# Kernel optimization log

Hardware: AMD Instinct MI355X
Metric: run time of the kernel (lower is better)

## Reference

```python
import jax, jax.numpy as jnp
import numpy as np

P, U, R, C = 100000, 20000, 1000, 500
D, T, B = 64, 50, 4096
ET = 50000
NNZ_COL, NNZ_REG, NNZ_CAT, NNZ_T = 1_000_000, 300_000, 300_000, 1_000_000
N_LAYERS = 2


def setup_inputs() -> dict:
    key = jax.random.key(0)
    ks = iter(jax.random.split(key, 64))
    def nrm(shape, s=0.05):
        return (jax.random.normal(next(ks), shape, jnp.float32) * s)
    def ridx(n, hi):
        return jax.random.randint(next(ks), (n,), 0, hi, dtype=jnp.int32)
    def vals(n, scale):
        # roughly degree-normalized positive incidence weights
        return jax.random.uniform(next(ks), (n,), jnp.float32) * scale
    inp = {
        'user_idx': ridx(B, U),
        'user_seq': ridx((B, T)[0] * T, P + 1).reshape(B, T),
        'user_seq_mask': jax.random.randint(next(ks), (B, T), 0, 2, dtype=jnp.int32),
        'col_poi_idx': ridx(NNZ_COL, P), 'col_user_idx': ridx(NNZ_COL, U),
        'col_vals_pe': vals(NNZ_COL, 0.02), 'col_vals_ep': vals(NNZ_COL, 0.1),
        'reg_poi_idx': ridx(NNZ_REG, P), 'reg_region_idx': ridx(NNZ_REG, R),
        'reg_vals_pe': vals(NNZ_REG, 0.005), 'reg_vals_ep': vals(NNZ_REG, 0.3),
        'cat_poi_idx': ridx(NNZ_CAT, P), 'cat_cat_idx': ridx(NNZ_CAT, C),
        'cat_vals_pe': vals(NNZ_CAT, 0.003), 'cat_vals_ep': vals(NNZ_CAT, 0.3),
        'trans_poi_idx': ridx(NNZ_T, P), 'trans_edge_idx': ridx(NNZ_T, ET),
        'trans_vals_tar': vals(NNZ_T, 0.05), 'trans_vals_src': vals(NNZ_T, 0.1),
        'poi_emb': nrm((P + 1, D)), 'user_emb': nrm((U, D)),
        'region_emb': nrm((R, D)), 'cat_emb': nrm((C, D)),
        'w_gate_col': nrm((D, D)), 'b_gate_col': nrm((1, D)),
        'w_gate_trans': nrm((D, D)), 'b_gate_trans': nrm((1, D)),
        'w_gate_reg': nrm((D, D)), 'b_gate_reg': nrm((1, D)),
        'w_gate_cat': nrm((D, D)), 'b_gate_cat': nrm((1, D)),
        'col_Wp': nrm((D, D)), 'col_We': nrm((D, D)), 'col_Wf': nrm((2 * D, D)),
        'reg_Wp': nrm((D, D)), 'reg_We': nrm((D, D)), 'reg_Wf': nrm((2 * D, D)),
        'cat_Wp': nrm((D, D)), 'cat_We': nrm((D, D)), 'cat_Wf': nrm((2 * D, D)),
    }
    return inp


def _spmm(rows, cols, vals, X, n_rows):
    # sparse[n_rows, n_cols] @ X : gather source rows, scale, scatter-add to dest
    return jax.ops.segment_sum(vals[:, None] * X[cols], rows, num_segments=n_rows)


def _gate(x, W, b):
    return x * jax.nn.sigmoid(x @ W + b)


def _hetero_net(poi, edge, poi_idx, edge_idx, vals_pe, vals_ep, Wp, We, Wf, n_edge):
    # HG_poi_to_edge: rows=edge_idx, cols=poi_idx ; HG_edge_to_poi: rows=poi_idx, cols=edge_idx
    n_poi = poi.shape[0]
    acc_p, acc_e = poi, edge
    p, e = poi, edge
    for _ in range(N_LAYERS):
        poi_msg = _spmm(edge_idx, poi_idx, vals_pe, p @ Wp, n_edge)   # [n_edge, D]
        fused = jnp.concatenate([poi_msg, e @ We], axis=1) @ Wf       # [n_edge, D]
        prop = _spmm(poi_idx, edge_idx, vals_ep, fused, n_poi)        # [n_poi, D]
        p = prop + p      # residual (dropout p=0 -> identity)
        e = fused + e
        acc_p = acc_p + p
        acc_e = acc_e + e
    inv = 1.0 / (N_LAYERS + 1)
    return acc_p * inv, acc_e * inv


def _directed_net(poi, poi_idx, edge_idx, vals_tar, vals_src):
    n_poi = poi.shape[0]
    acc = poi
    p = poi
    for _ in range(N_LAYERS):
        msg_tar = _spmm(edge_idx, poi_idx, vals_tar, p, ET)       # HG_poi_tar @ p
        msg_src = _spmm(poi_idx, edge_idx, vals_src, msg_tar, n_poi)  # HG_poi_src @ msg_tar
        p = msg_src + p
        acc = acc + p
    return acc / (N_LAYERS + 1)


def _masked_mean(seq_embs, mask):
    m = mask.astype(seq_embs.dtype)[..., None]  # [B,T,1]
    denom = jnp.clip(m.sum(axis=1), 1.0)
    return (seq_embs * m).sum(axis=1) / denom


def reference(user_idx, user_seq, user_seq_mask,
              col_poi_idx, col_user_idx, col_vals_pe, col_vals_ep,
              reg_poi_idx, reg_region_idx, reg_vals_pe, reg_vals_ep,
              cat_poi_idx, cat_cat_idx, cat_vals_pe, cat_vals_ep,
              trans_poi_idx, trans_edge_idx, trans_vals_tar, trans_vals_src,
              poi_emb, user_emb, region_emb, cat_emb,
              w_gate_col, b_gate_col, w_gate_trans, b_gate_trans,
              w_gate_reg, b_gate_reg, w_gate_cat, b_gate_cat,
              col_Wp, col_We, col_Wf, reg_Wp, reg_We, reg_Wf,
              cat_Wp, cat_We, cat_Wf):
    base = poi_emb[:-1]  # drop padding row, [P, D]
    col_p = _gate(base, w_gate_col, b_gate_col)
    trans_p = _gate(base, w_gate_trans, b_gate_trans)
    reg_p = _gate(base, w_gate_reg, b_gate_reg)
    cat_p = _gate(base, w_gate_cat, b_gate_cat)

    col_poi_out, col_user_out = _hetero_net(col_p, user_emb, col_poi_idx, col_user_idx,
                                            col_vals_pe, col_vals_ep, col_Wp, col_We, col_Wf, U)
    reg_poi_out, _ = _hetero_net(reg_p, region_emb, reg_poi_idx, reg_region_idx,
                                 reg_vals_pe, reg_vals_ep, reg_Wp, reg_We, reg_Wf, R)
    cat_poi_out, _ = _hetero_net(cat_p, cat_emb, cat_poi_idx, cat_cat_idx,
                                 cat_vals_pe, cat_vals_ep, cat_Wp, cat_We, cat_Wf, C)
    trans_poi_out = _directed_net(trans_p, trans_poi_idx, trans_edge_idx,
                                  trans_vals_tar, trans_vals_src)

    zero = jnp.zeros((1, D), base.dtype)
    col_pad = jnp.concatenate([col_poi_out, zero], axis=0)
    reg_pad = jnp.concatenate([reg_poi_out, zero], axis=0)
    cat_pad = jnp.concatenate([cat_poi_out, zero], axis=0)
    trans_pad = jnp.concatenate([trans_poi_out, zero], axis=0)

    col_u = col_user_out[user_idx] + _masked_mean(col_pad[user_seq], user_seq_mask)
    reg_u = _masked_mean(reg_pad[user_seq], user_seq_mask)
    cat_u = _masked_mean(cat_pad[user_seq], user_seq_mask)
    trans_u = _masked_mean(trans_pad[user_seq], user_seq_mask)

    return jnp.stack([col_u, trans_u, reg_u, cat_u])  # [4, B, D]


if __name__ == '__main__':
    out = reference(**setup_inputs())
    print(out.shape, out.dtype)
```

## Files before the change

### kernel.cpp

```cpp
#include <hip/hip_runtime.h>

#define D 64
constexpr int Pn  = 100000;
constexpr int Un  = 20000;
constexpr int Rn  = 1000;
constexpr int Cn  = 500;
constexpr int Tn  = 50;
constexpr int Bn  = 4096;
constexpr int ETn = 50000;
constexpr int NNZ_COL = 1000000;
constexpr int NNZ_REG = 300000;
constexpr int NNZ_CAT = 300000;
constexpr int NNZ_T   = 1000000;
constexpr int STILE = 7040;
constexpr int NBMAX = 1024;
constexpr int CAP2 = 1536;
constexpr int NB2  = (Pn + 127) / 128;

static inline int cdiv(int a, int b) { return (a + b - 1) / b; }

__device__ __forceinline__ unsigned short f2bf(float f) {
  unsigned u = __float_as_uint(f);
  unsigned r = (u + 0x7FFF + ((u >> 16) & 1)) >> 16;
  return (unsigned short)r;
}
__device__ __forceinline__ float bflo(unsigned d) {
  return __uint_as_float(d << 16);
}
__device__ __forceinline__ float bfhi(unsigned d) {
  return __uint_as_float(d & 0xFFFF0000u);
}
__device__ __forceinline__ unsigned packbf(float a, float b) {
  return (unsigned)f2bf(a) | ((unsigned)f2bf(b) << 16);
}

struct SG {
  const int* k1; const int* o1; const float* v1;
  const int* k2; const int* o2; const float* v2;
  int2* sd; int* rowptr; int* cursorB;
  int s1, nb1, nk1, cap1, nblk, nnz, tile0, bkt0;
};
struct SG4 { SG g[4]; };

__global__ __launch_bounds__(256) void gate_kernel(
    const float* __restrict__ Xin, const float* __restrict__ W,
    const float* __restrict__ bias, unsigned short* __restrict__ P16,
    unsigned short* __restrict__ A16, int N) {
  __shared__ float sx[4][D];
  int tid = threadIdx.x, wv = tid >> 6, lane = tid & 63;
  float wcol[D];
#pragma unroll
  for (int k = 0; k < D; ++k) wcol[k] = W[k * D + lane];
  float bl = bias[lane];
  for (int row = blockIdx.x * 4 + wv; row < N; row += gridDim.x * 4) {
    float x = Xin[row * D + lane];
    sx[wv][lane] = x;
    float y = 0.f;
#pragma unroll
    for (int k = 0; k < D; ++k) y += sx[wv][k] * wcol[k];
    float s = 1.f / (1.f + __expf(-(y + bl)));
    float o = x * s;
    unsigned short ob = f2bf(o);
    P16[row * D + lane] = ob;
    A16[row * D + lane] = ob;
  }
}

__global__ __launch_bounds__(256) void matmul_kernel(
    const float* __restrict__ Xin, const float* __restrict__ W,
    float* __restrict__ Y, int N) {
  __shared__ float sx[4][D];
  int tid = threadIdx.x, wv = tid >> 6, lane = tid & 63;
  float wcol[D];
#pragma unroll
  for (int k = 0; k < D; ++k) wcol[k] = W[k * D + lane];
  for (int row = blockIdx.x * 4 + wv; row < N; row += gridDim.x * 4) {
    sx[wv][lane] = Xin[row * D + lane];
    float y = 0.f;
#pragma unroll
    for (int k = 0; k < D; ++k) y += sx[wv][k] * wcol[k];
    Y[row * D + lane] = y;
  }
}

__global__ __launch_bounds__(256) void fused2_resid_kernel(
    const float* __restrict__ A, const float* __restrict__ W1,
    const float* __restrict__ W2, unsigned short* __restrict__ fusedOut16,
    float* __restrict__ e_buf, float* __restrict__ accE, int N) {
  __shared__ float sa[4][D], sb2[4][D];
  int tid = threadIdx.x, wv = tid >> 6, lane = tid & 63;
  float w1[D], w2[D];
#pragma unroll
  for (int k = 0; k < D; ++k) {
    w1[k] = W1[k * D + lane];
    w2[k] = W2[k * D + lane];
  }
  for (int row = blockIdx.x * 4 + wv; row < N; row += gridDim.x * 4) {
    sa[wv][lane]  = A[row * D + lane];
    float eo = e_buf[row * D + lane];
    sb2[wv][lane] = eo;
    float y = 0.f;
#pragma unroll
    for (int k = 0; k < D; ++k) y += sa[wv][k] * w1[k] + sb2[wv][k] * w2[k];
    fusedOut16[row * D + lane] = f2bf(y);
    float en = eo + y;
    e_buf[row * D + lane] = en;
    accE[row * D + lane] += en;
  }
}

__global__ __launch_bounds__(256) void cursor_init_b_kernel(SG4 gs, int totb) {
  int b = blockIdx.x * blockDim.x + threadIdx.x;
  if (b >= totb) return;
  int gi = 3;
  while (gi > 0 && b < gs.g[gi].bkt0) --gi;
  const SG& g = gs.g[gi];
  int lb = b - g.bkt0;
  g.cursorB[lb] =
      (lb < g.nb1) ? lb * g.cap1 : g.nb1 * g.cap1 + (lb - g.nb1) * CAP2;
}

__global__ __launch_bounds__(1024) void scatter_b_kernel(SG4 gs) {
  extern __shared__ int ls[];
  int2* stage = (int2*)ls;
  int* lcnt   = ls;
  int* lbase  = ls + 2 * STILE;
  int* gbase  = lbase + (NBMAX + 1);
  __shared__ int wsum[17];
  int b = blockIdx.x;
  int gi = 3;
  while (gi > 0 && b < gs.g[gi].tile0) --gi;
  const SG& g = gs.g[gi];
  int t = b - g.tile0;
  bool d2 = t >= g.nblk;
  const int* kk = d2 ? g.k2 : g.k1;
  const int* oo = d2 ? g.o2 : g.o1;
  const float* vv = d2 ? g.v2 : g.v1;
  int sft = d2 ? 7 : g.s1;
  int kb = d2 ? g.nb1 : 0;
  int nb = d2 ? NB2 : g.nb1;
  int msk = (1 << sft) - 1;
  int tile = d2 ? t - g.nblk : t;
  int tid = threadIdx.x;
  for (int k = tid; k < nb; k += 1024) lcnt[k] = 0;
  __syncthreads();
  int t0 = tile * STILE, t1 = min(t0 + STILE, g.nnz);
  int fill = t1 - t0;
  int key[7], off[7], ox[7], vx[7];
#pragma unroll
  for (int j = 0; j < 7; ++j) {
    int i = t0 + j * 1024 + tid;
    if (i < t1) {
      int r = kk[i];
      key[j] = r >> sft;
      ox[j] = ((r & msk) << 17) | oo[i];
      vx[j] = __float_as_int(vv[i]);
      off[j] = atomicAdd(&lcnt[key[j]], 1);
    } else {
      key[j] = -1; off[j] = 0; ox[j] = 0; vx[j] = 0;
    }
  }
  __syncthreads();
  {
    int lane = tid & 63, wv = tid >> 6;
    int c = (tid < nb) ? lcnt[tid] : 0;
    int sc = c;
#pragma unroll
    for (int d = 1; d < 64; d <<= 1) {
      int y = __shfl_up(sc, d);
      if (lane >= d) sc += y;
    }
    if (lane == 63) wsum[wv] = sc;
    __syncthreads();
    if (tid < 16) {
      int w = wsum[tid];
#pragma unroll
      for (int d = 1; d < 16; d <<= 1) {
        int y = __shfl_up(w, d);
        if (lane >= d) w += y;
      }
      wsum[tid] = w;
    }
    __syncthreads();
    int woff = (wv == 0) ? 0 : wsum[wv - 1];
    if (tid < nb) {
      lbase[tid] = woff + sc - c;
      gbase[tid] = c ? atomicAdd(&g.cursorB[kb + tid], c) : 0;
    }
    if (tid == 0) lbase[nb] = fill;
  }
  __syncthreads();
#pragma unroll
  for (int j = 0; j < 7; ++j)
    if (key[j] >= 0) stage[lbase[key[j]] + off[j]] = make_int2(ox[j], vx[j]);
  __syncthreads();
  for (int i = tid; i < fill; i += 1024) {
    int lo = 0, hi = nb;
    while (hi - lo > 1) {
      int mid = (lo + hi) >> 1;
      if (lbase[mid] <= i) lo = mid; else hi = mid;
    }
    g.sd[gbase[lo] + (i - lbase[lo])] = stage[i];
  }
}

__global__ __launch_bounds__(256) void refine_b_kernel(SG4 gs) {
  __shared__ int cnt[128];
  __shared__ int wsum[2];
  int bg = blockIdx.x;
  int gi = 3;
  while (gi > 0 && bg < gs.g[gi].bkt0) --gi;
  const SG& g = gs.g[gi];
  int b = bg - g.bkt0;
  int tid = threadIdx.x;
  int sft, row0, kbase, klim, bstart;
  if (b < g.nb1) {
    sft = g.s1; row0 = b << g.s1; kbase = 0; klim = g.nk1;
    bstart = b * g.cap1;
  } else {
    sft = 7; row0 = (b - g.nb1) << 7; kbase = g.nk1; klim = Pn;
    bstart = g.nb1 * g.cap1 + (b - g.nb1) * CAP2;
  }
  int rows = min(1 << sft, klim - row0);
  int bend = g.cursorB[b];
  if (rows == 1) {
    if (tid == 0) g.rowptr[kbase + row0] = bstart;
    return;
  }
  if (tid < rows) cnt[tid] = 0;
  __syncthreads();
  int2 st[8];
#pragma unroll
  for (int j = 0; j < 8; ++j) {
    int i = bstart + tid + (j << 8);
    st[j] = (i < bend) ? g.sd[i] : make_int2(0, 0);
  }
#pragma unroll
  for (int j = 0; j < 8; ++j) {
    int i = bstart + tid + (j << 8);
    if (i < bend) atomicAdd(&cnt[st[j].x >> 17], 1);
  }
  __syncthreads();
  int v = 0, sc = 0;
  if (tid < 128) {
    v = (tid < rows) ? cnt[tid] : 0;
    sc = v;
    int lane = tid & 63;
#pragma unroll
    for (int d = 1; d < 64; d <<= 1) {
      int y = __shfl_up(sc, d);
      if (lane >= d) sc += y;
    }
    if (lane == 63) wsum[tid >> 6] = sc;
  }
  __syncthreads();
  int excl = sc - v + ((tid >= 64 && tid < 128) ? wsum[0] : 0);
  __syncthreads();
  if (tid < rows) {
    g.rowptr[kbase + row0 + tid] = bstart + excl;
    cnt[tid] = excl;
  }
  __syncthreads();
#pragma unroll
  for (int j = 0; j < 8; ++j) {
    int i = bstart + tid + (j << 8);
    if (i < bend) {
      int r = st[j].x >> 17;
      int dst = bstart + atomicAdd(&cnt[r], 1);
      g.sd[dst] = st[j];
    }
  }
}

__global__ __launch_bounds__(256) void spmm_csr_kernel(
    const int* __restrict__ rowptr, const int* __restrict__ bEnd, int base,
    int nkx, int sft, int boff, const int2* __restrict__ sd,
    const uint4* __restrict__ X128, float* __restrict__ Yf,
    uint4* __restrict__ Y128, uint4* __restrict__ p128,
    uint4* __restrict__ a128, int nrows) {
  int lane = threadIdx.x & 63;
  int q = lane >> 3, l3 = lane & 7;
  int w = (int)((blockIdx.x * (long)blockDim.x + threadIdx.x) >> 6);
  if (w >= nrows) return;
  int idx = base + w;
  int start = rowptr[idx];
  int be = bEnd[boff + (w >> sft)];
  int end = (idx + 1 < nkx) ? min(rowptr[idx + 1], be) : be;
  float a0 = 0.f, a1 = 0.f, a2 = 0.f, a3 = 0.f;
  float a4 = 0.f, a5 = 0.f, a6 = 0.f, a7 = 0.f;
  float b0 = 0.f, b1 = 0.f, b2 = 0.f, b3 = 0.f;
  float b4 = 0.f, b5 = 0.f, b6 = 0.f, b7 = 0.f;
  int n = start + q;
  for (; n + 8 < end; n += 16) {
    int2 c0 = sd[n], c1 = sd[n + 8];
    uint4 d0 = X128[(size_t)(c0.x & 0x1FFFF) * 8 + l3];
    uint4 d1 = X128[(size_t)(c1.x & 0x1FFFF) * 8 + l3];
    float v0 = __int_as_float(c0.y), v1 = __int_as_float(c1.y);
    a0 += v0 * bflo(d0.x); a1 += v0 * bfhi(d0.x);
    a2 += v0 * bflo(d0.y); a3 += v0 * bfhi(d0.y);
    a4 += v0 * bflo(d0.z); a5 += v0 * bfhi(d0.z);
    a6 += v0 * bflo(d0.w); a7 += v0 * bfhi(d0.w);
    b0 += v1 * bflo(d1.x); b1 += v1 * bfhi(d1.x);
    b2 += v1 * bflo(d1.y); b3 += v1 * bfhi(d1.y);
    b4 += v1 * bflo(d1.z); b5 += v1 * bfhi(d1.z);
    b6 += v1 * bflo(d1.w); b7 += v1 * bfhi(d1.w);
  }
  for (; n < end; n += 8) {
    int2 cv = sd[n];
    uint4 dv = X128[(size_t)(cv.x & 0x1FFFF) * 8 + l3];
    float v = __int_as_float(cv.y);
    a0 += v * bflo(dv.x); a1 += v * bfhi(dv.x);
    a2 += v * bflo(dv.y); a3 += v * bfhi(dv.y);
    a4 += v * bflo(dv.z); a5 += v * bfhi(dv.z);
    a6 += v * bflo(dv.w); a7 += v * bfhi(dv.w);
  }
  float y0 = a0 + b0, y1 = a1 + b1, y2 = a2 + b2, y3 = a3 + b3;
  float y4 = a4 + b4, y5 = a5 + b5, y6 = a6 + b6, y7 = a7 + b7;
#pragma unroll
  for (int m = 8; m <= 32; m <<= 1) {
    y0 += __shfl(y0, lane ^ m); y1 += __shfl(y1, lane ^ m);
    y2 += __shfl(y2, lane ^ m); y3 += __shfl(y3, lane ^ m);
    y4 += __shfl(y4, lane ^ m); y5 += __shfl(y5, lane ^ m);
    y6 += __shfl(y6, lane ^ m); y7 += __shfl(y7, lane ^ m);
  }
  if (lane >= 8) return;
  size_t o = (size_t)w * 8 + l3;
  if (p128) {
    uint4 pv = p128[o];
    float p0 = bflo(pv.x) + y0, p1 = bfhi(pv.x) + y1;
    float p2 = bflo(pv.y) + y2, p3 = bfhi(pv.y) + y3;
    float p4 = bflo(pv.z) + y4, p5 = bfhi(pv.z) + y5;
    float p6 = bflo(pv.w) + y6, p7 = bfhi(pv.w) + y7;
    uint4 pn;
    pn.x = packbf(p0, p1); pn.y = packbf(p2, p3);
    pn.z = packbf(p4, p5); pn.w = packbf(p6, p7);
    p128[o] = pn;
    uint4 av = a128[o];
    uint4 an;
    an.x = packbf(bflo(av.x) + p0, bfhi(av.x) + p1);
    an.y = packbf(bflo(av.y) + p2, bfhi(av.y) + p3);
    an.z = packbf(bflo(av.z) + p4, bfhi(av.z) + p5);
    an.w = packbf(bflo(av.w) + p6, bfhi(av.w) + p7);
    a128[o] = an;
  } else if (Y128) {
    uint4 pk;
    pk.x = packbf(y0, y1); pk.y = packbf(y2, y3);
    pk.z = packbf(y4, y5); pk.w = packbf(y6, y7);
    Y128[o] = pk;
  } else {
    float4 lo; lo.x = y0; lo.y = y1; lo.z = y2; lo.w = y3;
    float4 hi; hi.x = y4; hi.y = y5; hi.z = y6; hi.w = y7;
    *(float4*)&Yf[(size_t)w * D + 8 * l3] = lo;
    *(float4*)&Yf[(size_t)w * D + 8 * l3 + 4] = hi;
  }
}

__global__ __launch_bounds__(256) void copy2_kernel(
    const float4* __restrict__ s, float4* __restrict__ a,
    float4* __restrict__ b, int n4) {
  int i = blockIdx.x * blockDim.x + threadIdx.x;
  if (i < n4) {
    float4 v = s[i];
    a[i] = v;
    b[i] = v;
  }
}

__global__ __launch_bounds__(256) void final_kernel(
    const int* __restrict__ user_idx, const int* __restrict__ seq,
    const int* __restrict__ mask, const uint2* __restrict__ colP16,
    const uint2* __restrict__ transP16, const uint2* __restrict__ regP16,
    const uint2* __restrict__ catP16, const float* __restrict__ colU,
    float* __restrict__ out) {
  int lane = threadIdx.x & 63;
  int q = lane >> 4, l4 = lane & 15;
  int wid = (int)((blockIdx.x * (long)blockDim.x + threadIdx.x) >> 6);
  if (wid >= Bn) return;
  float c0 = 0.f, c1 = 0.f, c2 = 0.f, c3 = 0.f;
  float t0 = 0.f, t1 = 0.f, t2 = 0.f, t3 = 0.f;
  float r0 = 0.f, r1 = 0.f, r2 = 0.f, r3 = 0.f;
  float g0 = 0.f, g1 = 0.f, g2 = 0.f, g3 = 0.f;
  int cnt = 0;
  for (int t = q; t < Tn; t += 4) {
    int m = mask[wid * Tn + t];
    int idx = seq[wid * Tn + t];
    cnt += m;
    if (m && idx < Pn) {
      size_t ro = (size_t)idx * 16 + l4;
      uint2 dc = colP16[ro];
      uint2 dt = transP16[ro];
      uint2 dr = regP16[ro];
      uint2 dg = catP16[ro];
      c0 += bflo(dc.x); c1 += bfhi(dc.x); c2 += bflo(dc.y); c3 += bfhi(dc.y);
      t0 += bflo(dt.x); t1 += bfhi(dt.x); t2 += bflo(dt.y); t3 += bfhi(dt.y);
      r0 += bflo(dr.x); r1 += bfhi(dr.x); r2 += bflo(dr.y); r3 += bfhi(dr.y);
      g0 += bflo(dg.x); g1 += bfhi(dg.x); g2 += bflo(dg.y); g3 += bfhi(dg.y);
    }
  }
  cnt += __shfl(cnt, lane ^ 16); cnt += __shfl(cnt, lane ^ 32);
  c0 += __shfl(c0, lane ^ 16); c0 += __shfl(c0, lane ^ 32);
  c1 += __shfl(c1, lane ^ 16); c1 += __shfl(c1, lane ^ 32);
  c2 += __shfl(c2, lane ^ 16); c2 += __shfl(c2, lane ^ 32);
  c3 += __shfl(c3, lane ^ 16); c3 += __shfl(c3, lane ^ 32);
  t0 += __shfl(t0, lane ^ 16); t0 += __shfl(t0, lane ^ 32);
  t1 += __shfl(t1, lane ^ 16); t1 += __shfl(t1, lane ^ 32);
  t2 += __shfl(t2, lane ^ 16); t2 += __shfl(t2, lane ^ 32);
  t3 += __shfl(t3, lane ^ 16); t3 += __shfl(t3, lane ^ 32);
  r0 += __shfl(r0, lane ^ 16); r0 += __shfl(r0, lane ^ 32);
  r1 += __shfl(r1, lane ^ 16); r1 += __shfl(r1, lane ^ 32);
  r2 += __shfl(r2, lane ^ 16); r2 += __shfl(r2, lane ^ 32);
  r3 += __shfl(r3, lane ^ 16); r3 += __shfl(r3, lane ^ 32);
  g0 += __shfl(g0, lane ^ 16); g0 += __shfl(g0, lane ^ 32);
  g1 += __shfl(g1, lane ^ 16); g1 += __shfl(g1, lane ^ 32);
  g2 += __shfl(g2, lane ^ 16); g2 += __shfl(g2, lane ^ 32);
  g3 += __shfl(g3, lane ^ 16); g3 += __shfl(g3, lane ^ 32);
  if (lane >= 16) return;
  float dn = 1.f / (float)(cnt > 0 ? cnt : 1);
  const float inv = 1.f / 3.f;
  int u = user_idx[wid];
  float4 cu = *(const float4*)&colU[(size_t)u * D + 4 * l4];
  size_t ob = (size_t)wid * D + 4 * l4;
  float4 o0;
  o0.x = (cu.x + c0 * dn) * inv; o0.y = (cu.y + c1 * dn) * inv;
  o0.z = (cu.z + c2 * dn) * inv; o0.w = (cu.w + c3 * dn) * inv;
  *(float4*)&out[0 * Bn * D + ob] = o0;
  float4 o1v;
  o1v.x = t0 * dn * inv; o1v.y = t1 * dn * inv;
  o1v.z = t2 * dn * inv; o1v.w = t3 * dn * inv;
  *(float4*)&out[1 * Bn * D + ob] = o1v;
  float4 o2v;
  o2v.x = r0 * dn * inv; o2v.y = r1 * dn * inv;
  o2v.z = r2 * dn * inv; o2v.w = r3 * dn * inv;
  *(float4*)&out[2 * Bn * D + ob] = o2v;
  float4 o3v;
  o3v.x = g0 * dn * inv; o3v.y = g1 * dn * inv;
  o3v.z = g2 * dn * inv; o3v.w = g3 * dn * inv;
  *(float4*)&out[3 * Bn * D + ob] = o3v;
}

extern "C" void kernel_launch(void* const* d_in, const int* in_sizes, int n_in,
                              void* d_out, int out_size, void* d_ws,
                              size_t ws_size, hipStream_t stream) {
  (void)in_sizes; (void)n_in; (void)out_size; (void)ws_size;
  const int*   user_idx      = (const int*)d_in[0];
  const int*   user_seq      = (const int*)d_in[1];
  const int*   user_seq_mask = (const int*)d_in[2];
  const int*   col_poi_idx   = (const int*)d_in[3];
  const int*   col_user_idx  = (const int*)d_in[4];
  const float* col_vals_pe   = (const float*)d_in[5];
  const float* col_vals_ep   = (const float*)d_in[6];
  const int*   reg_poi_idx   = (const int*)d_in[7];
  const int*   reg_region_idx= (const int*)d_in[8];
  const float* reg_vals_pe   = (const float*)d_in[9];
  const float* reg_vals_ep   = (const float*)d_in[10];
  const int*   cat_poi_idx   = (const int*)d_in[11];
  const int*   cat_cat_idx   = (const int*)d_in[12];
  const float* cat_vals_pe   = (const float*)d_in[13];
  const float* cat_vals_ep   = (const float*)d_in[14];
  const int*   trans_poi_idx = (const int*)d_in[15];
  const int*   trans_edge_idx= (const int*)d_in[16];
  const float* trans_vals_tar= (const float*)d_in[17];
  const float* trans_vals_src= (const float*)d_in[18];
  const float* poi_emb       = (const float*)d_in[19];
  const float* user_emb      = (const float*)d_in[20];
  const float* region_emb    = (const float*)d_in[21];
  const float* cat_emb       = (const float*)d_in[22];
  const float* w_gate_col    = (const float*)d_in[23];
  const float* b_gate_col    = (const float*)d_in[24];
  const float* w_gate_trans  = (const float*)d_in[25];
  const float* b_gate_trans  = (const float*)d_in[26];
  const float* w_gate_reg    = (const float*)d_in[27];
  const float* b_gate_reg    = (const float*)d_in[28];
  const float* w_gate_cat    = (const float*)d_in[29];
  const float* b_gate_cat    = (const float*)d_in[30];
  const float* col_Wp = (const float*)d_in[31];
  const float* col_We = (const float*)d_in[32];
  const float* col_Wf = (const float*)d_in[33];
  const float* reg_Wp = (const float*)d_in[34];
  const float* reg_We = (const float*)d_in[35];
  const float* reg_Wf = (const float*)d_in[36];
  const float* cat_Wp = (const float*)d_in[37];
  const float* cat_We = (const float*)d_in[38];
  const float* cat_Wf = (const float*)d_in[39];

  float* ws = (float*)d_ws;
  size_t off = 0;
  auto alloc = [&](size_t n) { float* p = ws + off; off += n; return p; };
  const size_t PD = (size_t)Pn * D;
  const size_t UD = (size_t)Un * D;
  const size_t ED = (size_t)ETn * D;

  float* colU   = alloc(UD);
  float* e_buf  = alloc(UD);
  float* tmpE1  = alloc(UD);
  float* acce   = alloc((size_t)Rn * D);
  float* WpWf   = alloc(D * D);
  float* WeWf   = alloc(D * D);
  unsigned short* tmpE2_16 = (unsigned short*)alloc(UD / 2);
  unsigned short* tmpE1_16 = (unsigned short*)alloc(ED / 2);
  unsigned short* p16      = (unsigned short*)alloc(PD / 2);
  unsigned short* colP16   = (unsigned short*)alloc(PD / 2);
  unsigned short* regP16   = (unsigned short*)alloc(PD / 2);
  unsigned short* catP16   = (unsigned short*)alloc(PD / 2);
  unsigned short* transP16 = (unsigned short*)alloc(PD / 2);

  const int s1_[4]   = {5, 0, 0, 6};
  const int nk1_[4]  = {Un, Rn, Cn, ETn};
  const int cap1_[4] = {2048, 512, 1024, 1536};
  const int nnz_[4]  = {NNZ_COL, NNZ_REG, NNZ_CAT, NNZ_T};
  SG4 gs;
  int tile0 = 0, bkt0 = 0;
  size_t sdoff = 0, rpoff = 0;
  int2* sdbase;
  int *rpbase, *curbase;
  {
    size_t sdtot = 0;
    for (int i = 0; i < 4; ++i) {
      int nb1 = cdiv(nk1_[i], 1 << s1_[i]);
      sdtot += (size_t)nb1 * cap1_[i] + (size_t)NB2 * CAP2;
    }
    sdbase = (int2*)alloc(2 * sdtot);
    rpbase = (int*)alloc(Un + Rn + Cn + ETn + 4 * Pn + 8);
    curbase = (int*)alloc(4 * 2048);
  }
  const int* k1s[4] = {col_user_idx, reg_region_idx, cat_cat_idx,
                       trans_edge_idx};
  const int* o1s[4] = {col_poi_idx, reg_poi_idx, cat_poi_idx, trans_poi_idx};
  const float* v1s[4] = {col_vals_pe, reg_vals_pe, cat_vals_pe,
                         trans_vals_tar};
  const float* v2s[4] = {col_vals_ep, reg_vals_ep, cat_vals_ep,
                         trans_vals_src};
  for (int i = 0; i < 4; ++i) {
    SG& g = gs.g[i];
    g.k1 = k1s[i]; g.o1 = o1s[i]; g.v1 = v1s[i];
    g.k2 = o1s[i]; g.o2 = k1s[i]; g.v2 = v2s[i];
    g.s1 = s1_[i]; g.nk1 = nk1_[i]; g.cap1 = cap1_[i]; g.nnz = nnz_[i];
    g.nb1 = cdiv(g.nk1, 1 << g.s1);
    g.nblk = cdiv(g.nnz, STILE);
    g.sd = sdbase + sdoff;
    g.rowptr = rpbase + rpoff;
    g.cursorB = curbase + i * 2048;
    g.tile0 = tile0; g.bkt0 = bkt0;
    sdoff += (size_t)g.nb1 * g.cap1 + (size_t)NB2 * CAP2;
    rpoff += g.nk1 + Pn;
    tile0 += 2 * g.nblk;
    bkt0 += g.nb1 + NB2;
  }
  int tottiles = tile0, totbkt = bkt0;

  cursor_init_b_kernel<<<cdiv(totbkt, 256), 256, 0, stream>>>(gs, totbkt);
  scatter_b_kernel<<<tottiles, 1024, (2 * STILE + 2 * NBMAX + 1) * 4,
                     stream>>>(gs);
  refine_b_kernel<<<totbkt, 256, 0, stream>>>(gs);

  const int GCAP = 1024;

  auto spmm = [&](const SG& g, int base, int sft, int boff,
                  const unsigned short* X16, float* Yf, unsigned short* Y16,
                  unsigned short* prmw, unsigned short* armw, int nrows) {
    spmm_csr_kernel<<<cdiv(nrows, 4), 256, 0, stream>>>(
        g.rowptr, g.cursorB, base, g.nk1 + Pn, sft, boff, g.sd,
        (const uint4*)X16, Yf, (uint4*)Y16, (uint4*)prmw, (uint4*)armw,
        nrows);
  };

  auto hetero = [&](int gi, const float* wg, const float* bg,
                    const float* edge_emb, int Ne, const float* Wp,
                    const float* We, const float* Wf, float* accE,
                    unsigned short* acc16) {
    const SG& g = gs.g[gi];
    gate_kernel<<<GCAP, 256, 0, stream>>>(poi_emb, wg, bg, p16, acc16, Pn);
    copy2_kernel<<<cdiv(Ne * D / 4, 256), 256, 0, stream>>>(
        (const float4*)edge_emb, (float4*)e_buf, (float4*)accE, Ne * D / 4);
    matmul_kernel<<<16, 256, 0, stream>>>(Wp, Wf, WpWf, D);
    matmul_kernel<<<16, 256, 0, stream>>>(We, Wf + D * D, WeWf, D);
    for (int l = 0; l < 2; ++l) {
      spmm(g, 0, g.s1, 0, p16, tmpE1, nullptr, nullptr, nullptr, Ne);
      fused2_resid_kernel<<<min(cdiv(Ne, 4), GCAP), 256, 0, stream>>>(
          tmpE1, WpWf, WeWf, tmpE2_16, e_buf, accE, Ne);
      spmm(g, g.nk1, 7, g.nb1, tmpE2_16, nullptr, nullptr, p16, acc16, Pn);
    }
  };

  hetero(0, w_gate_col, b_gate_col, user_emb, Un, col_Wp, col_We, col_Wf,
         colU, colP16);
  hetero(1, w_gate_reg, b_gate_reg, region_emb, Rn, reg_Wp, reg_We, reg_Wf,
         acce, regP16);
  hetero(2, w_gate_cat, b_gate_cat, cat_emb, Cn, cat_Wp, cat_We, cat_Wf,
         acce, catP16);

  {
    const SG& g = gs.g[3];
    gate_kernel<<<GCAP, 256, 0, stream>>>(poi_emb, w_gate_trans, b_gate_trans,
                                          p16, transP16, Pn);
    for (int l = 0; l < 2; ++l) {
      spmm(g, 0, g.s1, 0, p16, nullptr, tmpE1_16, nullptr, nullptr, ETn);
      spmm(g, g.nk1, 7, g.nb1, tmpE1_16, nullptr, nullptr, p16, transP16, Pn);
    }
  }

  final_kernel<<<cdiv(Bn * 64, 256), 256, 0, stream>>>(
      user_idx, user_seq, user_seq_mask, (const uint2*)colP16,
      (const uint2*)transP16, (const uint2*)regP16, (const uint2*)catP16,
      colU, (float*)d_out);
}
```

Before: 766.9 us.

## Batch gate and weight-product kernels, skip accumulator update on first layer

Merges the four separate gate launches into a single kernel where each wavefront applies a different gate to shared rows of poi_emb, so the POI embedding table is read once rather than four times. The six weight-product matmuls are combined into one launch. The accumulator read-modify-write in the second SpMM is dropped on layer 0 and applied algebraically on layer 1 as acc + q + p, removing one full bf16 pass over the POI accumulator per network. This needs four separate P buffers and changes the bf16 rounding order of the accumulator sum.

```diff
diff --git a/kernel.cpp b/kernel.cpp
--- a/kernel.cpp
+++ b/kernel.cpp
@@ -42,45 +42,60 @@
 };
 struct SG4 { SG g[4]; };
 
-__global__ __launch_bounds__(256) void gate_kernel(
-    const float* __restrict__ Xin, const float* __restrict__ W,
-    const float* __restrict__ bias, unsigned short* __restrict__ P16,
-    unsigned short* __restrict__ A16, int N) {
+struct G4 {
+  const float* W[4]; const float* b[4];
+  unsigned short* P[4]; unsigned short* A[4];
+};
+
+struct W6 { const float* A[6]; const float* Bm[6]; float* O[6]; };
+
+__global__ __launch_bounds__(256) void gate4_kernel(G4 g,
+                                                   const float* __restrict__ X,
+                                                   int N) {
   __shared__ float sx[4][D];
   int tid = threadIdx.x, wv = tid >> 6, lane = tid & 63;
   float wcol[D];
-#pragma unroll
-  for (int k = 0; k < D; ++k) wcol[k] = W[k * D + lane];
-  float bl = bias[lane];
-  for (int row = blockIdx.x * 4 + wv; row < N; row += gridDim.x * 4) {
-    float x = Xin[row * D + lane];
-    sx[wv][lane] = x;
-    float y = 0.f;
-#pragma unroll
-    for (int k = 0; k < D; ++k) y += sx[wv][k] * wcol[k];
-    float s = 1.f / (1.f + __expf(-(y + bl)));
-    float o = x * s;
-    unsigned short ob = f2bf(o);
-    P16[row * D + lane] = ob;
-    A16[row * D + lane] = ob;
-  }
-}
-
-__global__ __launch_bounds__(256) void matmul_kernel(
-    const float* __restrict__ Xin, const float* __restrict__ W,
-    float* __restrict__ Y, int N) {
+  const float* Wg = g.W[wv];
+#pragma unroll
+  for (int k = 0; k < D; ++k) wcol[k] = Wg[k * D + lane];
+  float bl = g.b[wv][lane];
+  unsigned short* Pw = g.P[wv];
+  unsigned short* Aw = g.A[wv];
+  for (int row0 = blockIdx.x * 4; row0 < N; row0 += gridDim.x * 4) {
+    sx[wv][lane] = X[(size_t)(row0 + wv) * D + lane];
+    __syncthreads();
+#pragma unroll
+    for (int r = 0; r < 4; ++r) {
+      float y = 0.f;
+#pragma unroll
+      for (int k = 0; k < D; ++k) y += sx[r][k] * wcol[k];
+      float x = sx[r][lane];
+      float s = 1.f / (1.f + __expf(-(y + bl)));
+      unsigned short ob = f2bf(x * s);
+      size_t o = (size_t)(row0 + r) * D + lane;
+      Pw[o] = ob;
+      Aw[o] = ob;
+    }
+    __syncthreads();
+  }
+}
+
+__global__ __launch_bounds__(256) void wprod_kernel(W6 w) {
   __shared__ float sx[4][D];
   int tid = threadIdx.x, wv = tid >> 6, lane = tid & 63;
+  int p = blockIdx.x >> 4, blk = blockIdx.x & 15;
+  const float* A = w.A[p];
+  const float* Bm = w.Bm[p];
+  float* O = w.O[p];
   float wcol[D];
 #pragma unroll
-  for (int k = 0; k < D; ++k) wcol[k] = W[k * D + lane];
-  for (int row = blockIdx.x * 4 + wv; row < N; row += gridDim.x * 4) {
-    sx[wv][lane] = Xin[row * D + lane];
-    float y = 0.f;
-#pragma unroll
-    for (int k = 0; k < D; ++k) y += sx[wv][k] * wcol[k];
-    Y[row * D + lane] = y;
-  }
+  for (int k = 0; k < D; ++k) wcol[k] = Bm[k * D + lane];
+  int row = blk * 4 + wv;
+  sx[wv][lane] = A[row * D + lane];
+  float y = 0.f;
+#pragma unroll
+  for (int k = 0; k < D; ++k) y += sx[wv][k] * wcol[k];
+  O[row * D + lane] = y;
 }
 
 __global__ __launch_bounds__(256) void fused2_resid_kernel(
@@ -327,21 +342,25 @@
   size_t o = (size_t)w * 8 + l3;
   if (p128) {
     uint4 pv = p128[o];
-    float p0 = bflo(pv.x) + y0, p1 = bfhi(pv.x) + y1;
-    float p2 = bflo(pv.y) + y2, p3 = bfhi(pv.y) + y3;
-    float p4 = bflo(pv.z) + y4, p5 = bfhi(pv.z) + y5;
-    float p6 = bflo(pv.w) + y6, p7 = bfhi(pv.w) + y7;
+    float q0 = bflo(pv.x), q1 = bfhi(pv.x);
+    float q2 = bflo(pv.y), q3 = bfhi(pv.y);
+    float q4 = bflo(pv.z), q5 = bfhi(pv.z);
+    float q6 = bflo(pv.w), q7 = bfhi(pv.w);
+    float p0 = q0 + y0, p1 = q1 + y1, p2 = q2 + y2, p3 = q3 + y3;
+    float p4 = q4 + y4, p5 = q5 + y5, p6 = q6 + y6, p7 = q7 + y7;
     uint4 pn;
     pn.x = packbf(p0, p1); pn.y = packbf(p2, p3);
     pn.z = packbf(p4, p5); pn.w = packbf(p6, p7);
     p128[o] = pn;
-    uint4 av = a128[o];
-    uint4 an;
-    an.x = packbf(bflo(av.x) + p0, bfhi(av.x) + p1);
-    an.y = packbf(bflo(av.y) + p2, bfhi(av.y) + p3);
-    an.z = packbf(bflo(av.z) + p4, bfhi(av.z) + p5);
-    an.w = packbf(bflo(av.w) + p6, bfhi(av.w) + p7);
-    a128[o] = an;
+    if (a128) {
+      uint4 av = a128[o];
+      uint4 an;
+      an.x = packbf(bflo(av.x) + q0 + p0, bfhi(av.x) + q1 + p1);
+      an.y = packbf(bflo(av.y) + q2 + p2, bfhi(av.y) + q3 + p3);
+      an.z = packbf(bflo(av.z) + q4 + p4, bfhi(av.z) + q5 + p5);
+      an.w = packbf(bflo(av.w) + q6 + p6, bfhi(av.w) + q7 + p7);
+      a128[o] = an;
+    }
   } else if (Y128) {
     uint4 pk;
     pk.x = packbf(y0, y1); pk.y = packbf(y2, y3);
@@ -494,11 +513,13 @@
   float* e_buf  = alloc(UD);
   float* tmpE1  = alloc(UD);
   float* acce   = alloc((size_t)Rn * D);
-  float* WpWf   = alloc(D * D);
-  float* WeWf   = alloc(D * D);
+  float* Wbuf   = alloc(6 * D * D);
   unsigned short* tmpE2_16 = (unsigned short*)alloc(UD / 2);
   unsigned short* tmpE1_16 = (unsigned short*)alloc(ED / 2);
-  unsigned short* p16      = (unsigned short*)alloc(PD / 2);
+  unsigned short* p16_0    = (unsigned short*)alloc(PD / 2);
+  unsigned short* p16_1    = (unsigned short*)alloc(PD / 2);
+  unsigned short* p16_2    = (unsigned short*)alloc(PD / 2);
+  unsigned short* p16_3    = (unsigned short*)alloc(PD / 2);
   unsigned short* colP16   = (unsigned short*)alloc(PD / 2);
   unsigned short* regP16   = (unsigned short*)alloc(PD / 2);
   unsigned short* catP16   = (unsigned short*)alloc(PD / 2);
@@ -548,6 +569,22 @@
   }
   int tottiles = tile0, totbkt = bkt0;
 
+  W6 w6;
+  w6.A[0] = col_Wp; w6.Bm[0] = col_Wf;          w6.O[0] = Wbuf + 0 * D * D;
+  w6.A[1] = col_We; w6.Bm[1] = col_Wf + D * D;  w6.O[1] = Wbuf + 1 * D * D;
+  w6.A[2] = reg_Wp; w6.Bm[2] = reg_Wf;          w6.O[2] = Wbuf + 2 * D * D;
+  w6.A[3] = reg_We; w6.Bm[3] = reg_Wf + D * D;  w6.O[3] = Wbuf + 3 * D * D;
+  w6.A[4] = cat_Wp; w6.Bm[4] = cat_Wf;          w6.O[4] = Wbuf + 4 * D * D;
+  w6.A[5] = cat_We; w6.Bm[5] = cat_Wf + D * D;  w6.O[5] = Wbuf + 5 * D * D;
+  wprod_kernel<<<96, 256, 0, stream>>>(w6);
+
+  G4 g4;
+  g4.W[0] = w_gate_col;   g4.b[0] = b_gate_col;   g4.P[0] = p16_0; g4.A[0] = colP16;
+  g4.W[1] = w_gate_reg;   g4.b[1] = b_gate_reg;   g4.P[1] = p16_1; g4.A[1] = regP16;
+  g4.W[2] = w_gate_cat;   g4.b[2] = b_gate_cat;   g4.P[2] = p16_2; g4.A[2] = catP16;
+  g4.W[3] = w_gate_trans; g4.b[3] = b_gate_trans; g4.P[3] = p16_3; g4.A[3] = transP16;
+  gate4_kernel<<<1024, 256, 0, stream>>>(g4, poi_emb, Pn);
+
   cursor_init_b_kernel<<<cdiv(totbkt, 256), 256, 0, stream>>>(gs, totbkt);
   scatter_b_kernel<<<tottiles, 1024, (2 * STILE + 2 * NBMAX + 1) * 4,
                      stream>>>(gs);
@@ -564,38 +601,32 @@
         nrows);
   };
 
-  auto hetero = [&](int gi, const float* wg, const float* bg,
-                    const float* edge_emb, int Ne, const float* Wp,
-                    const float* We, const float* Wf, float* accE,
-                    unsigned short* acc16) {
+  auto hetero = [&](int gi, const float* edge_emb, int Ne, float* accE,
+                    unsigned short* p16, unsigned short* acc16) {
     const SG& g = gs.g[gi];
-    gate_kernel<<<GCAP, 256, 0, stream>>>(poi_emb, wg, bg, p16, acc16, Pn);
+    const float* WpWf = Wbuf + (2 * gi) * D * D;
+    const float* WeWf = Wbuf + (2 * gi + 1) * D * D;
     copy2_kernel<<<cdiv(Ne * D / 4, 256), 256, 0, stream>>>(
         (const float4*)edge_emb, (float4*)e_buf, (float4*)accE, Ne * D / 4);
-    matmul_kernel<<<16, 256, 0, stream>>>(Wp, Wf, WpWf, D);
-    matmul_kernel<<<16, 256, 0, stream>>>(We, Wf + D * D, WeWf, D);
     for (int l = 0; l < 2; ++l) {
       spmm(g, 0, g.s1, 0, p16, tmpE1, nullptr, nullptr, nullptr, Ne);
       fused2_resid_kernel<<<min(cdiv(Ne, 4), GCAP), 256, 0, stream>>>(
           tmpE1, WpWf, WeWf, tmpE2_16, e_buf, accE, Ne);
-      spmm(g, g.nk1, 7, g.nb1, tmpE2_16, nullptr, nullptr, p16, acc16, Pn);
+      spmm(g, g.nk1, 7, g.nb1, tmpE2_16, nullptr, nullptr, p16,
+           (l == 1) ? acc16 : nullptr, Pn);
     }
   };
 
-  hetero(0, w_gate_col, b_gate_col, user_emb, Un, col_Wp, col_We, col_Wf,
-         colU, colP16);
-  hetero(1, w_gate_reg, b_gate_reg, region_emb, Rn, reg_Wp, reg_We, reg_Wf,
-         acce, regP16);
-  hetero(2, w_gate_cat, b_gate_cat, cat_emb, Cn, cat_Wp, cat_We, cat_Wf,
-         acce, catP16);
+  hetero(0, user_emb, Un, colU, p16_0, colP16);
+  hetero(1, region_emb, Rn, acce, p16_1, regP16);
+  hetero(2, cat_emb, Cn, acce, p16_2, catP16);
 
   {
     const SG& g = gs.g[3];
-    gate_kernel<<<GCAP, 256, 0, stream>>>(poi_emb, w_gate_trans, b_gate_trans,
-                                          p16, transP16, Pn);
     for (int l = 0; l < 2; ++l) {
-      spmm(g, 0, g.s1, 0, p16, nullptr, tmpE1_16, nullptr, nullptr, ETn);
-      spmm(g, g.nk1, 7, g.nb1, tmpE1_16, nullptr, nullptr, p16, transP16, Pn);
+      spmm(g, 0, g.s1, 0, p16_3, nullptr, tmpE1_16, nullptr, nullptr, ETn);
+      spmm(g, g.nk1, 7, g.nb1, tmpE1_16, nullptr, nullptr, p16_3,
+           (l == 1) ? transP16 : nullptr, Pn);
     }
   }
 
```

Result: faster. 730.6 us (-4.7%).
